# Kernel tuning notes

Hardware: AMD Instinct MI355X
Metric: run time of the kernel (lower is better)

The kernel has to match this reference:

```python
import jax, jax.numpy as jnp
import numpy as np

K = 3
DILATION = 1
DG = 1  # deformable groups


def _deform_conv2d(x, offsets, mask, weight, bias, k=K, dilation=DILATION, dg=DG):
    # x: [B, C, H, W]; offsets: [B, dg*2*k*k, H, W]; mask: [B, dg*k*k, H, W]
    # weight: [O, C, k, k]; bias: [O]
    B, C, H, W = x.shape
    O = weight.shape[0]
    Cg = C // dg
    kk = k * k
    pad = (k // 2) * dilation

    # base sampling grid per kernel tap (stride=1)
    ky, kx = jnp.meshgrid(jnp.arange(k), jnp.arange(k), indexing='ij')
    ky = ky.reshape(kk)
    kx = kx.reshape(kk)
    base_y = (jnp.arange(H)[None, :, None] - pad + ky[:, None, None] * dilation)  # [kk,H,1]
    base_x = (jnp.arange(W)[None, None, :] - pad + kx[:, None, None] * dilation)  # [kk,1,W]

    off = offsets.reshape(B, dg, kk, 2, H, W)
    py = base_y[None, None].astype(x.dtype) + off[:, :, :, 0]  # [B,dg,kk,H,W]
    px = base_x[None, None].astype(x.dtype) + off[:, :, :, 1]  # [B,dg,kk,H,W]

    y0 = jnp.floor(py)
    x0 = jnp.floor(px)
    wy1 = py - y0  # frac weights
    wx1 = px - x0
    wy0 = 1.0 - wy1
    wx0 = 1.0 - wx1

    img = x.reshape(B, dg, Cg, H * W)

    def gather(yi, xi):
        # yi, xi: float integer-valued coords [B,dg,kk,H,W]; zero outside bounds
        valid = (yi >= 0) & (yi <= H - 1) & (xi >= 0) & (xi <= W - 1)
        yc = jnp.clip(yi, 0, H - 1).astype(jnp.int32)
        xc = jnp.clip(xi, 0, W - 1).astype(jnp.int32)
        idx = (yc * W + xc).reshape(B, dg, 1, kk * H * W)
        vals = jnp.take_along_axis(img, idx, axis=3).reshape(B, dg, Cg, kk, H, W)
        return vals * valid.reshape(B, dg, 1, kk, H, W).astype(x.dtype)

    def w5(a):  # lift [B,dg,kk,H,W] -> [B,dg,1,kk,H,W]
        return a.reshape(B, dg, 1, kk, H, W)

    sampled = (gather(y0, x0) * w5(wy0 * wx0)
               + gather(y0, x0 + 1) * w5(wy0 * wx1)
               + gather(y0 + 1, x0) * w5(wy1 * wx0)
               + gather(y0 + 1, x0 + 1) * w5(wy1 * wx1))  # [B,dg,Cg,kk,H,W]

    sampled = sampled * mask.reshape(B, dg, 1, kk, H, W)
    sampled = sampled.reshape(B, C, kk, H, W)

    out = jnp.einsum('bckhw,ock->bohw', sampled, weight.reshape(O, C, kk))
    return out + bias[None, :, None, None]


def setup_inputs() -> dict:
    key = jax.random.key(0)
    k1, k2, k3, k4, k5 = jax.random.split(key, 5)
    B, C, O, H, W = 8, 128, 128, 64, 64
    x = jax.random.normal(k1, (B, C, H, W), dtype=jnp.float32)
    offsets = jax.random.normal(k2, (B, DG * 2 * K * K, H, W), dtype=jnp.float32)
    mask = jax.random.uniform(k3, (B, DG * K * K, H, W), dtype=jnp.float32)
    fan_in = C * K * K
    weight = jax.random.normal(k4, (O, C, K, K), dtype=jnp.float32) / np.sqrt(fan_in)
    bias = jax.random.normal(k5, (O,), dtype=jnp.float32) * 0.01
    return {"x": x, "offsets": offsets, "mask": mask, "weight": weight, "bias": bias}


def reference(x, offsets, mask, weight, bias):
    return _deform_conv2d(x, offsets, mask, weight, bias)
```

## Files before the change

### kernel.cpp

```cpp
#include <hip/hip_runtime.h>
#include <math.h>

constexpr int Bn = 8, Cn = 128, On = 128, Hn = 64, Wn = 64;
constexpr int KK = 9, PAD = 1, BDIM = 256;
constexpr int PXB = 32;
constexpr int CG = 16;
constexpr int NG = Cn / CG;
constexpr int KG = 160;
constexpr int KTOT = NG * KG;
constexpr int BANDH = 10;
constexpr int XSTP = 657;
constexpr int AST = 170;
constexpr int ME = KK * PXB;

typedef __attribute__((ext_vector_type(8))) short bf16x8;
typedef __attribute__((ext_vector_type(4))) float f32x4;
typedef unsigned short u16;
typedef unsigned int u32;

__device__ inline u16 f2bf(float f) {
    union { float f; u32 u; } v; v.f = f;
    return (u16)((v.u + 0x7FFFu + ((v.u >> 16) & 1u)) >> 16);
}
__device__ inline u32 pk2bf(float a, float b) {
    return (u32)f2bf(a) | ((u32)f2bf(b) << 16);
}
__device__ inline float bflo(u32 w) { return __uint_as_float(w << 16); }
__device__ inline float bfhi(u32 w) { return __uint_as_float(w & 0xFFFF0000u); }

__global__ void wprep_kernel(const float* __restrict__ w, u16* __restrict__ wbf) {
    const int e = blockIdx.x * BDIM + threadIdx.x;
    const int o  = e / KTOT;
    const int kp = e - o * KTOT;
    const int g  = kp / KG;
    const int r  = kp - g * KG;
    const int t  = r >> 4;
    const int cl = r & 15;
    float v = 0.f;
    if (t < KK) v = w[o * (Cn * KK) + (g * CG + cl) * KK + t];
    wbf[e] = f2bf(v);
}

__global__ __launch_bounds__(BDIM, 4)
void dcn_mfma_kernel(const float* __restrict__ x,
                     const float* __restrict__ offs,
                     const float* __restrict__ mask,
                     const u16*   __restrict__ wbf,
                     const float* __restrict__ bias,
                     float* __restrict__ out)
{
    __shared__ __align__(16) u32 pband[8 * XSTP];
    __shared__ __align__(16) u16 ash[PXB * AST];

    const int tid    = threadIdx.x;
    const int b      = blockIdx.x & 7;
    const int rem    = blockIdx.x >> 3;
    const int h      = rem >> 1;
    const int pxbase = (rem & 1) * PXB;
    const int r0     = min(max(h - 4, 0), Hn - BANDH);

    const int s_px4  = tid & 15;
    const int s_pair = (tid >> 4) & 7;
    float4 bnda[5], bndb[5];
    {
        #pragma unroll
        for (int it = 0; it < 5; ++it) {
            const int row = (tid + it * BDIM) >> 7;
            const float* base = x + (((size_t)(b * Cn + 2 * s_pair)) << 12)
                                + (r0 + row) * Wn + (s_px4 << 2);
            bnda[it] = *(const float4*)base;
            bndb[it] = *(const float4*)(base + 4096);
        }
    }

    float4 mw[2]; int2 mq[2]; int2 mi[2];
    #pragma unroll
    for (int it = 0; it < 2; ++it) {
        mw[it] = make_float4(0.f, 0.f, 0.f, 0.f);
        mq[it] = make_int2(r0 << 8, r0 << 8);
        mi[it] = make_int2(7, 7);
        const int e = tid + it * BDIM;
        if (e < ME) {
            const int t = e >> 5, px = e & 31, pg = pxbase + px;
            const int ty = t / 3, tx = t - ty * 3;
            const float oy = offs[((b * 18 + 2 * t    ) * Hn + h) * Wn + pg];
            const float ox = offs[((b * 18 + 2 * t + 1) * Hn + h) * Wn + pg];
            const float m  = mask[((b * KK + t) * Hn + h) * Wn + pg];
            const float py = (float)(h - PAD + ty) + oy;
            const float qx = (float)(pg - PAD + tx) + ox;
            const float fy = floorf(py), fx = floorf(qx);
            const float wy1 = py - fy, wx1 = qx - fx;
            const float wy0 = 1.f - wy1, wx0 = 1.f - wx1;
            const int y0 = (int)fy, x0 = (int)fx;
            const bool cx0 = (x0 >= 0) && (x0 < Wn);
            const bool cx1 = (x0 >= -1) && (x0 < Wn - 1);
            const float wr[2] = { wy0, wy1 };
            float wout[4]; int qout[2], iout[2];
            #pragma unroll
            for (int j = 0; j < 2; ++j) {
                const int yr = y0 + j;
                const bool rv = (yr >= 0) && (yr < Hn);
                wout[2 * j]     = (rv && cx0) ? wr[j] * wx0 * m : 0.f;
                wout[2 * j + 1] = (rv && cx1) ? wr[j] * wx1 * m : 0.f;
                int qv;
                if (!rv || (!cx0 && !cx1)) qv = r0 << 8;
                else                       qv = (yr << 8) | (x0 + 1);
                const bool inband = (qv >> 8) >= r0 && (qv >> 8) < r0 + BANDH;
                qout[j] = inband ? qv : ~qv;
                iout[j] = (((qv >> 8) - r0) << 6) + (qv & 255) + 7;
            }
            mw[it] = make_float4(wout[0], wout[1], wout[2], wout[3]);
            mq[it] = make_int2(qout[0], qout[1]);
            mi[it] = make_int2(iout[0], iout[1]);
        }
    }

    {
        #pragma unroll
        for (int it = 0; it < 5; ++it) {
            const int row = (tid + it * BDIM) >> 7;
            u32* d = &pband[s_pair * XSTP + row * 64 + 8 + (s_px4 << 2)];
            d[0] = pk2bf(bnda[it].x, bndb[it].x);
            d[1] = pk2bf(bnda[it].y, bndb[it].y);
            d[2] = pk2bf(bnda[it].z, bndb[it].z);
            d[3] = pk2bf(bnda[it].w, bndb[it].w);
        }
        if (tid < 128) {
            const int pr = tid >> 4, ws = tid & 15;
            pband[pr * XSTP + (ws < 8 ? ws : 640 + ws)] = 0;
        }
        ((u32*)ash)[(tid >> 3) * 85 + 72 + (tid & 7)] = 0;
    }
    __syncthreads();

    const int wv = tid >> 6, ln = tid & 63, quad = ln >> 4, l16 = ln & 15;
    const u16* wrow0 = wbf + (size_t)(wv * 32 + l16) * KTOT;

    f32x4 acc[2][2];
    #pragma unroll
    for (int mt = 0; mt < 2; ++mt)
        #pragma unroll
        for (int nt = 0; nt < 2; ++nt) acc[mt][nt] = (f32x4){0.f, 0.f, 0.f, 0.f};

    for (int g = 0; g < NG; ++g) {
        #pragma unroll
        for (int it = 0; it < 2; ++it) {
            const int e = tid + it * BDIM;
            if (e < ME) {
                const int t = e >> 5, px = e & 31;
                const float4 w  = mw[it];
                const int2   q  = mq[it];
                const int2   ix = mi[it];
                u32 avp[8];
                if (!__any((q.x | q.y) < 0)) {
                    #pragma unroll
                    for (int c2 = 0; c2 < 8; ++c2) {
                        const u32* pc = &pband[c2 * XSTP];
                        const u32 wt0 = pc[ix.x], wt1 = pc[ix.x + 1];
                        const u32 wb0 = pc[ix.y], wb1 = pc[ix.y + 1];
                        const float va = fmaf(w.x, bflo(wt0), fmaf(w.y, bflo(wt1),
                                         fmaf(w.z, bflo(wb0), w.w * bflo(wb1))));
                        const float vb = fmaf(w.x, bfhi(wt0), fmaf(w.y, bfhi(wt1),
                                         fmaf(w.z, bfhi(wb0), w.w * bfhi(wb1))));
                        avp[c2] = pk2bf(va, vb);
                    }
                } else {
                    const int qx = q.x < 0 ? ~q.x : q.x;
                    const int qy = q.y < 0 ? ~q.y : q.y;
                    const int yrx = qx >> 8, yry = qy >> 8;
                    const int xx = (qx & 255) - 1, xy = (qy & 255) - 1;
                    const int ax0 = max(xx, 0), ax1 = min(xx + 1, Wn - 1);
                    const int ay0 = max(xy, 0), ay1 = min(xy + 1, Wn - 1);
                    const float* gp = x + (((size_t)(b * Cn + g * CG)) << 12);
                    for (int c2 = 0; c2 < 8; ++c2) {
                        float v2[2];
                        for (int sb = 0; sb < 2; ++sb) {
                            const float* gc = gp + ((2 * c2 + sb) << 12);
                            const float t0 = gc[yrx * Wn + ax0], t1 = gc[yrx * Wn + ax1];
                            const float b0 = gc[yry * Wn + ay0], b1 = gc[yry * Wn + ay1];
                            v2[sb] = fmaf(w.x, t0, fmaf(w.y, t1,
                                     fmaf(w.z, b0, w.w * b1)));
                        }
                        avp[c2] = pk2bf(v2[0], v2[1]);
                    }
                }
                u32* d = (u32*)ash + px * 85 + t * 8;
                #pragma unroll
                for (int j = 0; j < 8; ++j) d[j] = avp[j];
            }
        }
        __syncthreads();

        if (g + 1 < NG) {
            #pragma unroll
            for (int it = 0; it < 5; ++it) {
                const int row = (tid + it * BDIM) >> 7;
                const float* base = x + (((size_t)(b * Cn + (g + 1) * CG + 2 * s_pair)) << 12)
                                    + (r0 + row) * Wn + (s_px4 << 2);
                bnda[it] = *(const float4*)base;
                bndb[it] = *(const float4*)(base + 4096);
            }
        }

        const u32* ad = (const u32*)ash;
        #pragma unroll
        for (int s = 0; s < 5; ++s) {
            const int kg = g * KG + s * 32 + quad * 8;
            const bf16x8 a0 = *(const bf16x8*)(wrow0 + kg);
            const bf16x8 a1 = *(const bf16x8*)(wrow0 + 16 * KTOT + kg);
            union BF { bf16x8 v; u32 w[4]; } b0, b1;
            const int kd = s * 16 + quad * 4;
            #pragma unroll
            for (int j = 0; j < 4; ++j) {
                b0.w[j] = ad[(0 * 16 + l16) * 85 + kd + j];
                b1.w[j] = ad[(1 * 16 + l16) * 85 + kd + j];
            }
            acc[0][0] = __builtin_amdgcn_mfma_f32_16x16x32_bf16(a0, b0.v, acc[0][0], 0, 0, 0);
            acc[0][1] = __builtin_amdgcn_mfma_f32_16x16x32_bf16(a0, b1.v, acc[0][1], 0, 0, 0);
            acc[1][0] = __builtin_amdgcn_mfma_f32_16x16x32_bf16(a1, b0.v, acc[1][0], 0, 0, 0);
            acc[1][1] = __builtin_amdgcn_mfma_f32_16x16x32_bf16(a1, b1.v, acc[1][1], 0, 0, 0);
        }

        if (g + 1 < NG) {
            #pragma unroll
            for (int it = 0; it < 5; ++it) {
                const int row = (tid + it * BDIM) >> 7;
                u32* d = &pband[s_pair * XSTP + row * 64 + 8 + (s_px4 << 2)];
                d[0] = pk2bf(bnda[it].x, bndb[it].x);
                d[1] = pk2bf(bnda[it].y, bndb[it].y);
                d[2] = pk2bf(bnda[it].z, bndb[it].z);
                d[3] = pk2bf(bnda[it].w, bndb[it].w);
            }
        }
        __syncthreads();
    }

    float* tr = (float*)pband;
    #pragma unroll
    for (int mt = 0; mt < 2; ++mt)
        #pragma unroll
        for (int nt = 0; nt < 2; ++nt)
            #pragma unroll
            for (int r = 0; r < 4; ++r) {
                const int o  = wv * 32 + mt * 16 + quad * 4 + r;
                const int px = nt * 16 + l16;
                tr[o * 36 + px] = acc[mt][nt][r] + bias[o];
            }
    __syncthreads();
    float* ob = out + (size_t)b * On * Hn * Wn + h * Wn + pxbase;
    {
        const int orow = tid >> 3, ck = tid & 7;
        #pragma unroll
        for (int it = 0; it < 4; ++it) {
            const int o = it * 32 + orow;
            const float4 v = *(const float4*)&tr[o * 36 + (ck << 2)];
            *(float4*)&ob[(size_t)o * (Hn * Wn) + (ck << 2)] = v;
        }
    }
}

constexpr int FB_PXB = 32, FB_CCH = 4, FB_NCT = FB_CCH * KK, FB_MW = KK * FB_PXB;

#define FMA4(A, S, W)                          \
    A.x = fmaf((S).x, (W), A.x);               \
    A.y = fmaf((S).y, (W), A.y);               \
    A.z = fmaf((S).z, (W), A.z);               \
    A.w = fmaf((S).w, (W), A.w);

__global__ __launch_bounds__(BDIM, 4)
void dcn_fb_kernel(const float* __restrict__ x,
                   const float* __restrict__ offs,
                   const float* __restrict__ mask,
                   const float* __restrict__ weight,
                   const float* __restrict__ bias,
                   float* __restrict__ out)
{
    __shared__ float wmeta[4 * FB_MW];
    __shared__ int   imeta[4 * FB_MW];
    __shared__ float ssh[FB_NCT * FB_PXB];
    __shared__ float wsh[FB_NCT * On];

    const int tid    = threadIdx.x;
    const int b      = blockIdx.x & 7;
    const int rem    = blockIdx.x >> 3;
    const int h      = rem >> 1;
    const int pxbase = (rem & 1) * FB_PXB;

    for (int e = tid; e < FB_MW; e += BDIM) {
        const int t  = e >> 5;
        const int px = e & 31;
        const int pg = pxbase + px;
        const int ty = t / 3, tx = t - ty * 3;
        const float oy = offs[((b * 18 + 2 * t    ) * Hn + h) * Wn + pg];
        const float ox = offs[((b * 18 + 2 * t + 1) * Hn + h) * Wn + pg];
        const float m  = mask[((b * KK + t) * Hn + h) * Wn + pg];
        const float py = (float)(h - PAD + ty) + oy;
        const float qx = (float)(pg - PAD + tx) + ox;
        const float y0 = floorf(py), x0 = floorf(qx);
        const float wy1 = py - y0, wx1 = qx - x0;
        const float wy0 = 1.f - wy1, wx0 = 1.f - wx1;
        const float cw[4] = { wy0 * wx0, wy0 * wx1, wy1 * wx0, wy1 * wx1 };
        #pragma unroll
        for (int k = 0; k < 4; ++k) {
            const float yk = y0 + (float)(k >> 1);
            const float xk = x0 + (float)(k & 1);
            const bool valid = (yk >= 0.f) && (yk <= (float)(Hn - 1)) &&
                               (xk >= 0.f) && (xk <= (float)(Wn - 1));
            const int yc = (int)fminf(fmaxf(yk, 0.f), (float)(Hn - 1));
            const int xc = (int)fminf(fmaxf(xk, 0.f), (float)(Wn - 1));
            wmeta[k * FB_MW + e] = valid ? cw[k] * m : 0.f;
            imeta[k * FB_MW + e] = yc * Wn + xc;
        }
    }
    __syncthreads();

    const int px0 = (tid & 7) << 2;
    const int oo  = (tid >> 3) << 2;

    float4 acc[4];
    #pragma unroll
    for (int j = 0; j < 4; ++j) acc[j] = make_float4(0.f, 0.f, 0.f, 0.f);

    for (int cb = 0; cb < Cn / FB_CCH; ++cb) {
        #pragma unroll
        for (int it = 0; it < (FB_NCT * On) / BDIM; ++it) {
            const int e = tid + it * BDIM;
            const int r = e >> 7;
            const int o = e & 127;
            wsh[r * On + o] = weight[o * (Cn * KK) + cb * FB_NCT + r];
        }
        for (int e = tid; e < FB_NCT * FB_PXB; e += BDIM) {
            const int px = e & 31;
            const int ct = e >> 5;
            const int c  = ct / 9;
            const int mb = (ct - c * 9) * FB_PXB + px;
            const float* xp = x + (((b * Cn) + cb * FB_CCH + c) << 12);
            float v =  wmeta[mb]              * xp[imeta[mb]];
            v = fmaf(wmeta[FB_MW     + mb], xp[imeta[FB_MW     + mb]], v);
            v = fmaf(wmeta[2 * FB_MW + mb], xp[imeta[2 * FB_MW + mb]], v);
            v = fmaf(wmeta[3 * FB_MW + mb], xp[imeta[3 * FB_MW + mb]], v);
            ssh[ct * FB_PXB + px] = v;
        }
        __syncthreads();

        #pragma unroll 6
        for (int ct = 0; ct < FB_NCT; ++ct) {
            const float4 sv = *(const float4*)&ssh[ct * FB_PXB + px0];
            const float4 wa = *(const float4*)&wsh[ct * On + oo];
            FMA4(acc[0], sv, wa.x);
            FMA4(acc[1], sv, wa.y);
            FMA4(acc[2], sv, wa.z);
            FMA4(acc[3], sv, wa.w);
        }
        __syncthreads();
    }

    #pragma unroll
    for (int j = 0; j < 4; ++j) {
        const float bv = bias[oo + j];
        float4 r = acc[j];
        r.x += bv; r.y += bv; r.z += bv; r.w += bv;
        *(float4*)&out[((b * On + oo + j) * Hn + h) * Wn + pxbase + px0] = r;
    }
}

extern "C" void kernel_launch(void* const* d_in, const int* in_sizes, int n_in,
                              void* d_out, int out_size, void* d_ws, size_t ws_size,
                              hipStream_t stream) {
    const float* x      = (const float*)d_in[0];
    const float* offs   = (const float*)d_in[1];
    const float* mask   = (const float*)d_in[2];
    const float* weight = (const float*)d_in[3];
    const float* bias   = (const float*)d_in[4];
    float* out = (float*)d_out;

    const size_t need = (size_t)On * KTOT * sizeof(u16);
    if (d_ws != nullptr && ws_size >= need) {
        u16* wbf = (u16*)d_ws;
        wprep_kernel<<<dim3(On * KTOT / BDIM), dim3(BDIM), 0, stream>>>(weight, wbf);
        dcn_mfma_kernel<<<dim3(Bn * Hn * 2), dim3(BDIM), 0, stream>>>(
            x, offs, mask, wbf, bias, out);
    } else {
        dcn_fb_kernel<<<dim3(Bn * Hn * 2), dim3(BDIM), 0, stream>>>(
            x, offs, mask, weight, bias, out);
    }
}
```

Measured before the change: 149.4 us.

## Process full rows per block with double-buffered sampling overlapped with MFMA

Each block now covers a whole 64-pixel row with 512 threads instead of half a row, which halves band loads per output pixel. The sampled-activation tile is double-buffered so sampling for the next channel group overlaps the MFMA steps of the current one, with band loads issued two groups ahead and weight fragments prefetched. It also uses the hardware packed bf16 convert instruction and rewrites the weight prep kernel to stage one output row in LDS. The cost is more LDS and registers per block and fewer blocks, which may lower occupancy.

Result: faster. 139.3 us (-6.8%).

```diff
diff --git a/kernel.cpp b/kernel.cpp
--- a/kernel.cpp
+++ b/kernel.cpp
@@ -2,43 +2,96 @@
 #include <math.h>
 
 constexpr int Bn = 8, Cn = 128, On = 128, Hn = 64, Wn = 64;
-constexpr int KK = 9, PAD = 1, BDIM = 256;
-constexpr int PXB = 32;
-constexpr int CG = 16;
-constexpr int NG = Cn / CG;
-constexpr int KG = 160;
-constexpr int KTOT = NG * KG;
-constexpr int BANDH = 10;
-constexpr int XSTP = 657;
-constexpr int AST = 170;
-constexpr int ME = KK * PXB;
+constexpr int KK = 9, PAD = 1;
+constexpr int BDIM = 512;
+constexpr int PXB  = 64;
+constexpr int CG = 16, NG = Cn / CG;
+constexpr int KG = 160, KTOT = NG * KG;
+constexpr int BANDH = 11;
+constexpr int XSTP = 716;
+constexpr int AST  = 81;
+constexpr int ME   = KK * PXB;
+constexpr int PB_DW  = 8 * XSTP;
+constexpr int ASH_DW = PXB * AST;
+constexpr int SM_DW  = PB_DW + 2 * ASH_DW;
+constexpr int BUNITS = BANDH * 128;
 
 typedef __attribute__((ext_vector_type(8))) short bf16x8;
 typedef __attribute__((ext_vector_type(4))) float f32x4;
 typedef unsigned short u16;
 typedef unsigned int u32;
 
-__device__ inline u16 f2bf(float f) {
+__device__ __forceinline__ u16 f2bf(float f) {
     union { float f; u32 u; } v; v.f = f;
     return (u16)((v.u + 0x7FFFu + ((v.u >> 16) & 1u)) >> 16);
 }
-__device__ inline u32 pk2bf(float a, float b) {
-    return (u32)f2bf(a) | ((u32)f2bf(b) << 16);
-}
-__device__ inline float bflo(u32 w) { return __uint_as_float(w << 16); }
-__device__ inline float bfhi(u32 w) { return __uint_as_float(w & 0xFFFF0000u); }
+__device__ __forceinline__ u32 cpk(float a, float b) {
+    u32 r;
+    asm("v_cvt_pk_bf16_f32 %0, %1, %2" : "=v"(r) : "v"(a), "v"(b));
+    return r;
+}
+__device__ __forceinline__ float bflo(u32 w) { return __uint_as_float(w << 16); }
+__device__ __forceinline__ float bfhi(u32 w) { return __uint_as_float(w & 0xFFFF0000u); }
 
 __global__ void wprep_kernel(const float* __restrict__ w, u16* __restrict__ wbf) {
-    const int e = blockIdx.x * BDIM + threadIdx.x;
-    const int o  = e / KTOT;
-    const int kp = e - o * KTOT;
-    const int g  = kp / KG;
-    const int r  = kp - g * KG;
-    const int t  = r >> 4;
-    const int cl = r & 15;
-    float v = 0.f;
-    if (t < KK) v = w[o * (Cn * KK) + (g * CG + cl) * KK + t];
-    wbf[e] = f2bf(v);
+    __shared__ u32 tmpw[KTOT / 2];
+    u16* tmp = (u16*)tmpw;
+    const int tid = threadIdx.x, o = blockIdx.x;
+    if (tid < 64)
+        tmpw[(tid >> 3) * 80 + 72 + (tid & 7)] = 0;
+    for (int k = tid; k < Cn * KK; k += 256) {
+        const int c = k / 9, t = k - 9 * c;
+        tmp[(c >> 4) * KG + t * 16 + (c & 15)] = f2bf(w[o * (Cn * KK) + k]);
+    }
+    __syncthreads();
+    u32* dst = (u32*)(wbf + (size_t)o * KTOT);
+    for (int e = tid; e < KTOT / 2; e += 256) dst[e] = tmpw[e];
+}
+
+__device__ __forceinline__ void do_sample(const u32* __restrict__ pband,
+                                          u32* __restrict__ ashW,
+                                          const float* __restrict__ xg,
+                                          const float4 w, const int2 q,
+                                          const int2 ix, const int e)
+{
+    const int t = e >> 6, px = e & 63;
+    u32 avp[8];
+    if (!__any((q.x | q.y) < 0)) {
+        const u32* p0 = pband + ix.x;
+        const u32* p1 = pband + ix.y;
+        #pragma unroll
+        for (int c2 = 0; c2 < 8; ++c2) {
+            const u32 wt0 = p0[c2 * XSTP], wt1 = p0[c2 * XSTP + 1];
+            const u32 wb0 = p1[c2 * XSTP], wb1 = p1[c2 * XSTP + 1];
+            const float va = fmaf(w.x, bflo(wt0), fmaf(w.y, bflo(wt1),
+                             fmaf(w.z, bflo(wb0), w.w * bflo(wb1))));
+            const float vb = fmaf(w.x, bfhi(wt0), fmaf(w.y, bfhi(wt1),
+                             fmaf(w.z, bfhi(wb0), w.w * bfhi(wb1))));
+            avp[c2] = cpk(va, vb);
+        }
+    } else {
+        const int qx = q.x < 0 ? ~q.x : q.x;
+        const int qy = q.y < 0 ? ~q.y : q.y;
+        const int yrx = qx >> 8, yry = qy >> 8;
+        const int xx = (qx & 255) - 1, xy = (qy & 255) - 1;
+        const int ax0 = max(xx, 0), ax1 = min(xx + 1, Wn - 1);
+        const int ay0 = max(xy, 0), ay1 = min(xy + 1, Wn - 1);
+        #pragma unroll
+        for (int c2 = 0; c2 < 8; ++c2) {
+            float v2[2];
+            #pragma unroll
+            for (int sb = 0; sb < 2; ++sb) {
+                const float* gc = xg + ((2 * c2 + sb) << 12);
+                const float t0 = gc[yrx * Wn + ax0], t1 = gc[yrx * Wn + ax1];
+                const float b0 = gc[yry * Wn + ay0], b1 = gc[yry * Wn + ay1];
+                v2[sb] = fmaf(w.x, t0, fmaf(w.y, t1, fmaf(w.z, b0, w.w * b1)));
+            }
+            avp[c2] = cpk(v2[0], v2[1]);
+        }
+    }
+    u32* d = ashW + px * AST + t * 8;
+    #pragma unroll
+    for (int j = 0; j < 8; ++j) d[j] = avp[j];
 }
 
 __global__ __launch_bounds__(BDIM, 4)
@@ -49,29 +102,43 @@
                      const float* __restrict__ bias,
                      float* __restrict__ out)
 {
-    __shared__ __align__(16) u32 pband[8 * XSTP];
-    __shared__ __align__(16) u16 ash[PXB * AST];
-
-    const int tid    = threadIdx.x;
-    const int b      = blockIdx.x & 7;
-    const int rem    = blockIdx.x >> 3;
-    const int h      = rem >> 1;
-    const int pxbase = (rem & 1) * PXB;
-    const int r0     = min(max(h - 4, 0), Hn - BANDH);
-
-    const int s_px4  = tid & 15;
-    const int s_pair = (tid >> 4) & 7;
-    float4 bnda[5], bndb[5];
-    {
-        #pragma unroll
-        for (int it = 0; it < 5; ++it) {
-            const int row = (tid + it * BDIM) >> 7;
-            const float* base = x + (((size_t)(b * Cn + 2 * s_pair)) << 12)
-                                + (r0 + row) * Wn + (s_px4 << 2);
-            bnda[it] = *(const float4*)base;
-            bndb[it] = *(const float4*)(base + 4096);
-        }
-    }
+    __shared__ __align__(16) u32 smem[SM_DW];
+    u32* const pband = smem;
+
+    const int tid = threadIdx.x;
+    const int b   = blockIdx.x & 7;
+    const int h   = blockIdx.x >> 3;
+    const int r0  = min(max(h - 5, 0), Hn - BANDH);
+
+    const int s_px4 = tid & 15, s_pair = (tid >> 4) & 7;
+
+    float4 bnda[3], bndb[3];
+#define BLOAD(GCH) { \
+        _Pragma("unroll") \
+        for (int it = 0; it < 3; ++it) { \
+            const int u = tid + it * BDIM; \
+            if (u < BUNITS) { \
+                const int row = u >> 7; \
+                const float* bp = x + (((size_t)(b * Cn + (GCH) * CG + 2 * s_pair)) << 12) \
+                                  + (r0 + row) * Wn + (s_px4 << 2); \
+                bnda[it] = *(const float4*)bp; \
+                bndb[it] = *(const float4*)(bp + 4096); \
+            } \
+        } }
+#define BWRITE() { \
+        _Pragma("unroll") \
+        for (int it = 0; it < 3; ++it) { \
+            const int u = tid + it * BDIM; \
+            if (u < BUNITS) { \
+                const int row = u >> 7; \
+                u32* d = &pband[s_pair * XSTP + row * 64 + 8 + (s_px4 << 2)]; \
+                *(uint4*)d = make_uint4( \
+                    cpk(bnda[it].x, bndb[it].x), cpk(bnda[it].y, bndb[it].y), \
+                    cpk(bnda[it].z, bndb[it].z), cpk(bnda[it].w, bndb[it].w)); \
+            } \
+        } }
+
+    BLOAD(0);
 
     float4 mw[2]; int2 mq[2]; int2 mi[2];
     #pragma unroll
@@ -81,13 +148,13 @@
         mi[it] = make_int2(7, 7);
         const int e = tid + it * BDIM;
         if (e < ME) {
-            const int t = e >> 5, px = e & 31, pg = pxbase + px;
+            const int t = e >> 6, px = e & 63;
             const int ty = t / 3, tx = t - ty * 3;
-            const float oy = offs[((b * 18 + 2 * t    ) * Hn + h) * Wn + pg];
-            const float ox = offs[((b * 18 + 2 * t + 1) * Hn + h) * Wn + pg];
-            const float m  = mask[((b * KK + t) * Hn + h) * Wn + pg];
+            const float oy = offs[((b * 18 + 2 * t    ) * Hn + h) * Wn + px];
+            const float ox = offs[((b * 18 + 2 * t + 1) * Hn + h) * Wn + px];
+            const float m  = mask[((b * KK + t) * Hn + h) * Wn + px];
             const float py = (float)(h - PAD + ty) + oy;
-            const float qx = (float)(pg - PAD + tx) + ox;
+            const float qx = (float)(px - PAD + tx) + ox;
             const float fy = floorf(py), fx = floorf(qx);
             const float wy1 = py - fy, wx1 = qx - fx;
             const float wy0 = 1.f - wy1, wx0 = 1.f - wx1;
@@ -115,150 +182,126 @@
         }
     }
 
+    if (tid < 128) {
+        const int pr = tid >> 4, ws = tid & 15;
+        if (ws < 12) pband[pr * XSTP + (ws < 8 ? ws : 704 + ws)] = 0;
+    }
+    #pragma unroll
+    for (int it = 0; it < 2; ++it) {
+        const int u = tid + it * BDIM;
+        smem[PB_DW + (u >> 9) * ASH_DW + ((u & 511) >> 3) * AST + 72 + (u & 7)] = 0;
+    }
+
+    BWRITE();
+    BLOAD(1);
+    __syncthreads();
+
+    const int wv = tid >> 6, ln = tid & 63, quad = ln >> 4, l16 = ln & 15;
+    const int mrow = wv >> 1, ncol = wv & 1;
+    const u16* wrow0 = wbf + (size_t)(mrow * 32 + l16) * KTOT;
+    const int npx0 = ncol * 32 + l16, npx1 = npx0 + 16;
+
     {
-        #pragma unroll
-        for (int it = 0; it < 5; ++it) {
-            const int row = (tid + it * BDIM) >> 7;
-            u32* d = &pband[s_pair * XSTP + row * 64 + 8 + (s_px4 << 2)];
-            d[0] = pk2bf(bnda[it].x, bndb[it].x);
-            d[1] = pk2bf(bnda[it].y, bndb[it].y);
-            d[2] = pk2bf(bnda[it].z, bndb[it].z);
-            d[3] = pk2bf(bnda[it].w, bndb[it].w);
-        }
-        if (tid < 128) {
-            const int pr = tid >> 4, ws = tid & 15;
-            pband[pr * XSTP + (ws < 8 ? ws : 640 + ws)] = 0;
-        }
-        ((u32*)ash)[(tid >> 3) * 85 + 72 + (tid & 7)] = 0;
+        const float* xg = x + (((size_t)(b * Cn)) << 12);
+        do_sample(pband, smem + PB_DW, xg, mw[0], mq[0], mi[0], tid);
+        if (tid < 64)
+            do_sample(pband, smem + PB_DW, xg, mw[1], mq[1], mi[1], BDIM + tid);
     }
     __syncthreads();
 
-    const int wv = tid >> 6, ln = tid & 63, quad = ln >> 4, l16 = ln & 15;
-    const u16* wrow0 = wbf + (size_t)(wv * 32 + l16) * KTOT;
-
     f32x4 acc[2][2];
     #pragma unroll
     for (int mt = 0; mt < 2; ++mt)
         #pragma unroll
         for (int nt = 0; nt < 2; ++nt) acc[mt][nt] = (f32x4){0.f, 0.f, 0.f, 0.f};
 
+    bf16x8 pa0[2], pa1[2];
+#define APRE(GG) { const int kgp = (GG) * KG + quad * 8; \
+        pa0[0] = *(const bf16x8*)(wrow0 + kgp); \
+        pa1[0] = *(const bf16x8*)(wrow0 + 16 * KTOT + kgp); \
+        pa0[1] = *(const bf16x8*)(wrow0 + kgp + 32); \
+        pa1[1] = *(const bf16x8*)(wrow0 + 16 * KTOT + kgp + 32); }
+    APRE(0);
+
+#define MSTEP_PRE(S) { \
+        union BF { bf16x8 v; u32 w[4]; } b0, b1; \
+        const int kd = (S) * 16 + quad * 4; \
+        _Pragma("unroll") \
+        for (int j = 0; j < 4; ++j) { \
+            b0.w[j] = ad[npx0 * AST + kd + j]; \
+            b1.w[j] = ad[npx1 * AST + kd + j]; \
+        } \
+        acc[0][0] = __builtin_amdgcn_mfma_f32_16x16x32_bf16(pa0[S], b0.v, acc[0][0], 0, 0, 0); \
+        acc[0][1] = __builtin_amdgcn_mfma_f32_16x16x32_bf16(pa0[S], b1.v, acc[0][1], 0, 0, 0); \
+        acc[1][0] = __builtin_amdgcn_mfma_f32_16x16x32_bf16(pa1[S], b0.v, acc[1][0], 0, 0, 0); \
+        acc[1][1] = __builtin_amdgcn_mfma_f32_16x16x32_bf16(pa1[S], b1.v, acc[1][1], 0, 0, 0); }
+
+#define MSTEP_LD(S) { \
+        const int kg = g * KG + (S) * 32 + quad * 8; \
+        const bf16x8 a0 = *(const bf16x8*)(wrow0 + kg); \
+        const bf16x8 a1 = *(const bf16x8*)(wrow0 + 16 * KTOT + kg); \
+        union BF { bf16x8 v; u32 w[4]; } b0, b1; \
+        const int kd = (S) * 16 + quad * 4; \
+        _Pragma("unroll") \
+        for (int j = 0; j < 4; ++j) { \
+            b0.w[j] = ad[npx0 * AST + kd + j]; \
+            b1.w[j] = ad[npx1 * AST + kd + j]; \
+        } \
+        acc[0][0] = __builtin_amdgcn_mfma_f32_16x16x32_bf16(a0, b0.v, acc[0][0], 0, 0, 0); \
+        acc[0][1] = __builtin_amdgcn_mfma_f32_16x16x32_bf16(a0, b1.v, acc[0][1], 0, 0, 0); \
+        acc[1][0] = __builtin_amdgcn_mfma_f32_16x16x32_bf16(a1, b0.v, acc[1][0], 0, 0, 0); \
+        acc[1][1] = __builtin_amdgcn_mfma_f32_16x16x32_bf16(a1, b1.v, acc[1][1], 0, 0, 0); }
+
     for (int g = 0; g < NG; ++g) {
-        #pragma unroll
-        for (int it = 0; it < 2; ++it) {
-            const int e = tid + it * BDIM;
-            if (e < ME) {
-                const int t = e >> 5, px = e & 31;
-                const float4 w  = mw[it];
-                const int2   q  = mq[it];
-                const int2   ix = mi[it];
-                u32 avp[8];
-                if (!__any((q.x | q.y) < 0)) {
-                    #pragma unroll
-                    for (int c2 = 0; c2 < 8; ++c2) {
-                        const u32* pc = &pband[c2 * XSTP];
-                        const u32 wt0 = pc[ix.x], wt1 = pc[ix.x + 1];
-                        const u32 wb0 = pc[ix.y], wb1 = pc[ix.y + 1];
-                        const float va = fmaf(w.x, bflo(wt0), fmaf(w.y, bflo(wt1),
-                                         fmaf(w.z, bflo(wb0), w.w * bflo(wb1))));
-                        const float vb = fmaf(w.x, bfhi(wt0), fmaf(w.y, bfhi(wt1),
-                                         fmaf(w.z, bfhi(wb0), w.w * bfhi(wb1))));
-                        avp[c2] = pk2bf(va, vb);
-                    }
-                } else {
-                    const int qx = q.x < 0 ? ~q.x : q.x;
-                    const int qy = q.y < 0 ? ~q.y : q.y;
-                    const int yrx = qx >> 8, yry = qy >> 8;
-                    const int xx = (qx & 255) - 1, xy = (qy & 255) - 1;
-                    const int ax0 = max(xx, 0), ax1 = min(xx + 1, Wn - 1);
-                    const int ay0 = max(xy, 0), ay1 = min(xy + 1, Wn - 1);
-                    const float* gp = x + (((size_t)(b * Cn + g * CG)) << 12);
-                    for (int c2 = 0; c2 < 8; ++c2) {
-                        float v2[2];
-                        for (int sb = 0; sb < 2; ++sb) {
-                            const float* gc = gp + ((2 * c2 + sb) << 12);
-                            const float t0 = gc[yrx * Wn + ax0], t1 = gc[yrx * Wn + ax1];
-                            const float b0 = gc[yry * Wn + ay0], b1 = gc[yry * Wn + ay1];
-                            v2[sb] = fmaf(w.x, t0, fmaf(w.y, t1,
-                                     fmaf(w.z, b0, w.w * b1)));
-                        }
-                        avp[c2] = pk2bf(v2[0], v2[1]);
-                    }
-                }
-                u32* d = (u32*)ash + px * 85 + t * 8;
-                #pragma unroll
-                for (int j = 0; j < 8; ++j) d[j] = avp[j];
-            }
-        }
+        const u32* ad = smem + PB_DW + (g & 1) * ASH_DW;
+        u32* ashN     = smem + PB_DW + ((g + 1) & 1) * ASH_DW;
+        if (g + 1 < NG) BWRITE();
+        MSTEP_PRE(0);
+        MSTEP_PRE(1);
         __syncthreads();
-
+        if (g + 2 < NG) BLOAD(g + 2);
         if (g + 1 < NG) {
-            #pragma unroll
-            for (int it = 0; it < 5; ++it) {
-                const int row = (tid + it * BDIM) >> 7;
-                const float* base = x + (((size_t)(b * Cn + (g + 1) * CG + 2 * s_pair)) << 12)
-                                    + (r0 + row) * Wn + (s_px4 << 2);
-                bnda[it] = *(const float4*)base;
-                bndb[it] = *(const float4*)(base + 4096);
-            }
-        }
-
-        const u32* ad = (const u32*)ash;
-        #pragma unroll
-        for (int s = 0; s < 5; ++s) {
-            const int kg = g * KG + s * 32 + quad * 8;
-            const bf16x8 a0 = *(const bf16x8*)(wrow0 + kg);
-            const bf16x8 a1 = *(const bf16x8*)(wrow0 + 16 * KTOT + kg);
-            union BF { bf16x8 v; u32 w[4]; } b0, b1;
-            const int kd = s * 16 + quad * 4;
-            #pragma unroll
-            for (int j = 0; j < 4; ++j) {
-                b0.w[j] = ad[(0 * 16 + l16) * 85 + kd + j];
-                b1.w[j] = ad[(1 * 16 + l16) * 85 + kd + j];
-            }
-            acc[0][0] = __builtin_amdgcn_mfma_f32_16x16x32_bf16(a0, b0.v, acc[0][0], 0, 0, 0);
-            acc[0][1] = __builtin_amdgcn_mfma_f32_16x16x32_bf16(a0, b1.v, acc[0][1], 0, 0, 0);
-            acc[1][0] = __builtin_amdgcn_mfma_f32_16x16x32_bf16(a1, b0.v, acc[1][0], 0, 0, 0);
-            acc[1][1] = __builtin_amdgcn_mfma_f32_16x16x32_bf16(a1, b1.v, acc[1][1], 0, 0, 0);
-        }
-
-        if (g + 1 < NG) {
-            #pragma unroll
-            for (int it = 0; it < 5; ++it) {
-                const int row = (tid + it * BDIM) >> 7;
-                u32* d = &pband[s_pair * XSTP + row * 64 + 8 + (s_px4 << 2)];
-                d[0] = pk2bf(bnda[it].x, bndb[it].x);
-                d[1] = pk2bf(bnda[it].y, bndb[it].y);
-                d[2] = pk2bf(bnda[it].z, bndb[it].z);
-                d[3] = pk2bf(bnda[it].w, bndb[it].w);
-            }
-        }
+            const float* xg = x + (((size_t)(b * Cn + (g + 1) * CG)) << 12);
+            do_sample(pband, ashN, xg, mw[0], mq[0], mi[0], tid);
+            if (tid < 64)
+                do_sample(pband, ashN, xg, mw[1], mq[1], mi[1], BDIM + tid);
+        }
+        MSTEP_LD(2);
+        MSTEP_LD(3);
+        MSTEP_LD(4);
+        if (g + 1 < NG) APRE(g + 1);
         __syncthreads();
     }
 
-    float* tr = (float*)pband;
+    float* tr = (float*)smem;
     #pragma unroll
     for (int mt = 0; mt < 2; ++mt)
         #pragma unroll
         for (int nt = 0; nt < 2; ++nt)
             #pragma unroll
             for (int r = 0; r < 4; ++r) {
-                const int o  = wv * 32 + mt * 16 + quad * 4 + r;
-                const int px = nt * 16 + l16;
-                tr[o * 36 + px] = acc[mt][nt][r] + bias[o];
+                const int o  = mrow * 32 + mt * 16 + quad * 4 + r;
+                const int px = ncol * 32 + nt * 16 + l16;
+                tr[o * 68 + px] = acc[mt][nt][r] + bias[o];
             }
     __syncthreads();
-    float* ob = out + (size_t)b * On * Hn * Wn + h * Wn + pxbase;
     {
-        const int orow = tid >> 3, ck = tid & 7;
+        const int orow = tid >> 2, f0 = tid & 3;
         #pragma unroll
         for (int it = 0; it < 4; ++it) {
-            const int o = it * 32 + orow;
-            const float4 v = *(const float4*)&tr[o * 36 + (ck << 2)];
-            *(float4*)&ob[(size_t)o * (Hn * Wn) + (ck << 2)] = v;
-        }
-    }
-}
-
+            const int f = f0 + it * 4;
+            const float4 v = *(const float4*)&tr[orow * 68 + (f << 2)];
+            *(float4*)&out[(((size_t)b * On + orow) * Hn + h) * Wn + (f << 2)] = v;
+        }
+    }
+#undef BLOAD
+#undef BWRITE
+#undef APRE
+#undef MSTEP_PRE
+#undef MSTEP_LD
+}
+
+constexpr int FBD = 256;
 constexpr int FB_PXB = 32, FB_CCH = 4, FB_NCT = FB_CCH * KK, FB_MW = KK * FB_PXB;
 
 #define FMA4(A, S, W)                          \
@@ -267,7 +310,7 @@
     A.z = fmaf((S).z, (W), A.z);               \
     A.w = fmaf((S).w, (W), A.w);
 
-__global__ __launch_bounds__(BDIM, 4)
+__global__ __launch_bounds__(FBD, 4)
 void dcn_fb_kernel(const float* __restrict__ x,
                    const float* __restrict__ offs,
                    const float* __restrict__ mask,
@@ -286,7 +329,7 @@
     const int h      = rem >> 1;
     const int pxbase = (rem & 1) * FB_PXB;
 
-    for (int e = tid; e < FB_MW; e += BDIM) {
+    for (int e = tid; e < FB_MW; e += FBD) {
         const int t  = e >> 5;
         const int px = e & 31;
         const int pg = pxbase + px;
@@ -323,13 +366,13 @@
 
     for (int cb = 0; cb < Cn / FB_CCH; ++cb) {
         #pragma unroll
-        for (int it = 0; it < (FB_NCT * On) / BDIM; ++it) {
-            const int e = tid + it * BDIM;
+        for (int it = 0; it < (FB_NCT * On) / FBD; ++it) {
+            const int e = tid + it * FBD;
             const int r = e >> 7;
             const int o = e & 127;
             wsh[r * On + o] = weight[o * (Cn * KK) + cb * FB_NCT + r];
         }
-        for (int e = tid; e < FB_NCT * FB_PXB; e += BDIM) {
+        for (int e = tid; e < FB_NCT * FB_PXB; e += FBD) {
             const int px = e & 31;
             const int ct = e >> 5;
             const int c  = ct / 9;
@@ -377,11 +420,11 @@
     const size_t need = (size_t)On * KTOT * sizeof(u16);
     if (d_ws != nullptr && ws_size >= need) {
         u16* wbf = (u16*)d_ws;
-        wprep_kernel<<<dim3(On * KTOT / BDIM), dim3(BDIM), 0, stream>>>(weight, wbf);
-        dcn_mfma_kernel<<<dim3(Bn * Hn * 2), dim3(BDIM), 0, stream>>>(
+        wprep_kernel<<<dim3(On), dim3(256), 0, stream>>>(weight, wbf);
+        dcn_mfma_kernel<<<dim3(Bn * Hn), dim3(BDIM), 0, stream>>>(
             x, offs, mask, wbf, bias, out);
     } else {
-        dcn_fb_kernel<<<dim3(Bn * Hn * 2), dim3(BDIM), 0, stream>>>(
+        dcn_fb_kernel<<<dim3(Bn * Hn * 2), dim3(FBD), 0, stream>>>(
             x, offs, mask, weight, bias, out);
     }
 }
```
